# Performance work log

Hardware: AMD Instinct MI355X
Metric: run time of the kernel (lower is better)

## Reference

```python
import jax, jax.numpy as jnp
import numpy as np
from jax import lax

FEAT_X, FEAT_Y = 50, 37          # generate_anchors(50, 37)
BASE_SIZE, DSR = 8.0, 16.0
A = FEAT_X * FEAT_Y * 9          # 16650 anchors


def generate_anchors():
    # Vectorized version of the triple python loop; order: x, y, size, [b1,b2,b3]
    xs = jnp.arange(FEAT_X, dtype=jnp.float32)[:, None, None]
    ys = jnp.arange(FEAT_Y, dtype=jnp.float32)[None, :, None]
    s = jnp.array([BASE_SIZE, 2 * BASE_SIZE, 4 * BASE_SIZE], jnp.float32)[None, None, :]

    def box(x1, y1, x2, y2):
        return jnp.stack(jnp.broadcast_arrays(x1 * DSR, y1 * DSR, x2 * DSR, y2 * DSR), axis=-1)

    b1 = box(xs - s / 2, ys - s / 2, xs + s / 2, ys + s / 2)      # square
    b2 = box(xs - s,     ys - s / 4, xs + s,     ys + s / 4)      # wide
    b3 = box(xs - s / 4, ys - s,     xs + s / 4, ys + s)          # tall
    anchors = jnp.stack([b1, b2, b3], axis=3)  # (50,37,3 sizes,3 variants,4)
    return anchors.reshape(-1, 4)              # (16650,4)


def conv2d(x, w, b, padding):
    y = lax.conv_general_dilated(x, w, (1, 1), padding,
                                 dimension_numbers=("NCHW", "OIHW", "NCHW"))
    return y + b[None, :, None, None]


def pairwise_iou(anchors, gt):
    # anchors: (A,4), gt: (B,G,4) -> iou (B,A,G); zero when no positive overlap
    a = anchors[None, :, None, :]
    g = gt[:, None, :, :]
    area_a = (a[..., 2] - a[..., 0]) * (a[..., 3] - a[..., 1])
    area_g = (g[..., 2] - g[..., 0]) * (g[..., 3] - g[..., 1])
    left = jnp.maximum(a[..., 0], g[..., 0])
    right = jnp.minimum(a[..., 2], g[..., 2])
    top = jnp.maximum(a[..., 1], g[..., 1])
    bot = jnp.minimum(a[..., 3], g[..., 3])
    no_ov = (left >= right) | (top >= bot)
    inter = jnp.where(no_ov, 0.0, (right - left) * (bot - top))
    return jnp.where(no_ov, 0.0, inter / (area_a + area_g - inter))


def setup_inputs() -> dict:
    key = jax.random.key(0)
    k1, k2, k3, k4, k5, k6, k7, k8 = jax.random.split(key, 8)
    B, G = 8, 20
    feats = jax.random.normal(k1, (B, 512, FEAT_Y, FEAT_X), jnp.float32)
    # well-formed gt boxes inside an ~800x592 image
    raw = jax.random.uniform(k2, (B, G, 2, 2)) * jnp.array([800.0, 592.0])
    x1y1 = jnp.min(raw, axis=2)
    x2y2 = jnp.max(raw, axis=2) + 1.0
    gt_boxes = jnp.concatenate([x1y1, x2y2], axis=-1)  # (B,G,4)
    im_info = jnp.array([[592.0, 800.0, 1.0]], jnp.float32)  # (h, w, scale)
    s = 0.02
    w3 = jax.random.normal(k3, (512, 512, 3, 3), jnp.float32) * s
    b3 = jnp.zeros((512,), jnp.float32)
    wc = jax.random.normal(k4, (18, 512, 1, 1), jnp.float32) * s
    bc = jnp.zeros((18,), jnp.float32)
    wb = jax.random.normal(k5, (36, 512, 1, 1), jnp.float32) * s
    bb = jnp.zeros((36,), jnp.float32)
    return {"feats": feats, "w3": w3, "b3": b3, "wc": wc, "bc": bc,
            "wb": wb, "bb": bb, "gt_boxes": gt_boxes, "im_info": im_info}


def reference(feats, w3, b3, wc, bc, wb, bb, gt_boxes, im_info):
    B = feats.shape[0]
    anchors = generate_anchors()
    rpn_conv1 = jax.nn.relu(conv2d(feats, w3, b3, ((1, 1), (1, 1))))
    rpn_cls_score = conv2d(rpn_conv1, wc, bc, ((0, 0), (0, 0)))  # (B,18,H,W)
    Bc, C, H, W = rpn_cls_score.shape
    score_rs = rpn_cls_score.reshape(Bc, 2, (C * H) // 2, W)      # reshape(x, 2)
    rpn_cls_prob = jax.nn.softmax(score_rs, axis=1).reshape(Bc, 18, H, W)
    rpn_bbox_pred = conv2d(rpn_conv1, wb, bb, ((0, 0), (0, 0)))   # (B,36,H,W)

    # anchor-target assignment (training branch), faithful to original logic
    inside = ((anchors[:, 0] >= 0) & (anchors[:, 1] >= 0) &
              (anchors[:, 2] < im_info[0, 1]) & (anchors[:, 3] < im_info[0, 0]))
    iou = pairwise_iou(anchors, gt_boxes)                 # (B,A,G)
    iou = jnp.where(inside[None, :, None], iou, 0.0)      # outside anchors skipped
    G = gt_boxes.shape[1]
    # original: idxs = argmax(iou_matrix[:][j]) with j == last gt index
    idx = jnp.argmax(iou[:, G - 1, :], axis=-1)           # (B,)
    labels = jnp.zeros((B, anchors.shape[0]), jnp.float32)
    labels = labels.at[jnp.arange(B), idx].set(1.0)
    max_iou = jnp.max(iou, axis=-1)                       # (B,A)
    labels = jnp.where(inside[None, :] & (max_iou > 0.7), 0.0, labels)

    out = jnp.concatenate([rpn_cls_prob, rpn_bbox_pred], axis=1)  # (B,54,H,W)
    return out, iou, labels
```

## Files before the change

### kernel.cpp

```cpp
#include <hip/hip_runtime.h>

typedef unsigned short u16;
typedef unsigned int u32;
typedef float f32x4 __attribute__((ext_vector_type(4)));
typedef short bf16x8 __attribute__((ext_vector_type(8)));

#define NB 8
#define FH 37
#define FW 50
#define FHW 1850
#define MTOT 14800
#define CIN 512
#define KTOT 4608
#define HP 39
#define WP 52
#define ANCH 16650
#define NG 20

__device__ __forceinline__ u16 f2bf(float f) {
    u32 u = __float_as_uint(f);
    u += 0x7fffu + ((u >> 16) & 1u);
    return (u16)(u >> 16);
}

__device__ __forceinline__ void gl2lds16(const u16* g, u16* l) {
    __builtin_amdgcn_global_load_lds((const __attribute__((address_space(1))) void*)(g),
                                     (__attribute__((address_space(3))) void*)(l),
                                     16, 0, 0);
}

__device__ __forceinline__ void anchor_box(int a, float& x1, float& y1, float& x2, float& y2) {
    int x = a / 333;
    int rem = a - x * 333;
    int y = rem / 9;
    int r2 = rem - y * 9;
    int si = r2 / 3;
    int bi = r2 - si * 3;
    float s = (float)(8 << si);
    float fx = (float)x, fy = (float)y;
    float ax1, ay1, ax2, ay2;
    if (bi == 0)      { float h = s * 0.5f;  ax1 = fx - h; ay1 = fy - h; ax2 = fx + h; ay2 = fy + h; }
    else if (bi == 1) { float q = s * 0.25f; ax1 = fx - s; ay1 = fy - q; ax2 = fx + s; ay2 = fy + q; }
    else              { float q = s * 0.25f; ax1 = fx - q; ay1 = fy - s; ax2 = fx + q; ay2 = fy + s; }
    x1 = ax1 * 16.f; y1 = ay1 * 16.f; x2 = ax2 * 16.f; y2 = ay2 * 16.f;
}

__global__ void k_prep(uint4* __restrict__ apad4, const float* __restrict__ w3,
                       u16* __restrict__ wt, const float* __restrict__ wc,
                       const float* __restrict__ wb, u16* __restrict__ whd) {
    int bx = blockIdx.x;
    int t = threadIdx.x;
    if (bx < 4056) {
        apad4[bx * 256 + t] = make_uint4(0u, 0u, 0u, 0u);
    } else if (bx < 13272) {
        int i = (bx - 4056) * 256 + t;
        int n = i / KTOT;
        int k = i - n * KTOT;
        int tap = k >> 9;
        int ci = k & 511;
        wt[i] = f2bf(w3[n * KTOT + ci * 9 + tap]);
    } else {
        int i = (bx - 13272) * 256 + t;
        int n = i >> 9;
        int ci = i & 511;
        float v = 0.f;
        if (n < 18) v = wc[n * 512 + ci];
        else if (n < 54) v = wb[(n - 18) * 512 + ci];
        whd[i] = f2bf(v);
    }
}

__global__ void k_transpose(const float* __restrict__ feats, u16* __restrict__ apad) {
    __shared__ float tile[32][33];
    int b  = blockIdx.z;
    int hw0 = blockIdx.x * 32;
    int c0  = blockIdx.y * 32;
    int tx = threadIdx.x, ty = threadIdx.y;
    int hw = hw0 + tx;
    if (hw < FHW) tile[ty][tx] = feats[(b * 512 + c0 + ty) * FHW + hw];
    __syncthreads();
    int hw2 = hw0 + ty;
    if (hw2 < FHW) {
        int h = hw2 / FW, w = hw2 - h * FW;
        apad[(((b * HP) + h + 1) * WP + (w + 1)) * 512 + c0 + tx] = f2bf(tile[tx][ty]);
    }
}

__global__ __launch_bounds__(256) void k_conv(const u16* __restrict__ apad,
                                              const u16* __restrict__ wt,
                                              const float* __restrict__ b3,
                                              u16* __restrict__ act) {
    __shared__ u16 As[128 * 64];
    __shared__ u16 Bs[64 * 64];
    int tid = threadIdx.x;
    int wave = tid >> 6, lane = tid & 63;
    int m0 = blockIdx.x * 128;
    int n0 = blockIdx.y * 64;
    int wr = wave >> 1, wn = wave & 1;
    int lm = lane & 15, lq = lane >> 4;
    int l7 = lm & 7;

    f32x4 acc[4][2] = {};

    int rloc = tid >> 3;
    int cg = (tid & 7) ^ (rloc & 7);
    int aBase[4], bBase[2];
    for (int i = 0; i < 4; i++) {
        int m = m0 + i * 32 + rloc; if (m > MTOT - 1) m = MTOT - 1;
        int b = m / FHW; int hw = m - b * FHW;
        int h = hw / FW; int w = hw - h * FW;
        aBase[i] = ((b * HP + h) * WP + w) * 512 + cg * 8;
    }
    for (int j = 0; j < 2; j++)
        bBase[j] = (n0 + j * 32 + rloc) * KTOT + cg * 8;

    u16* aL[4]; u16* bL[2];
    for (int i = 0; i < 4; i++) aL[i] = &As[(i * 32 + wave * 8) * 64];
    for (int j = 0; j < 2; j++) bL[j] = &Bs[(j * 32 + wave * 8) * 64];

    for (int kk = 0; kk < KTOT; kk += 64) {
        int tap = kk >> 9;
        int ci0 = kk & 511;
        int dy = tap / 3, dx = tap - dy * 3;
        int aOfs = (dy * WP + dx) * 512 + ci0;
        gl2lds16(apad + aBase[0] + aOfs, aL[0]);
        gl2lds16(apad + aBase[1] + aOfs, aL[1]);
        gl2lds16(apad + aBase[2] + aOfs, aL[2]);
        gl2lds16(apad + aBase[3] + aOfs, aL[3]);
        gl2lds16(wt + bBase[0] + kk, bL[0]);
        gl2lds16(wt + bBase[1] + kk, bL[1]);
        __syncthreads();
        bf16x8 a[2][4], b[2][2];
        #pragma unroll
        for (int ks = 0; ks < 2; ks++) {
            int slotb = ((ks * 4 + lq) ^ l7) * 8;
            #pragma unroll
            for (int i = 0; i < 4; i++)
                a[ks][i] = *(const bf16x8*)&As[(wr * 64 + i * 16 + lm) * 64 + slotb];
            #pragma unroll
            for (int j = 0; j < 2; j++)
                b[ks][j] = *(const bf16x8*)&Bs[(wn * 32 + j * 16 + lm) * 64 + slotb];
        }
        #pragma unroll
        for (int ks = 0; ks < 2; ks++)
            #pragma unroll
            for (int i = 0; i < 4; i++)
                #pragma unroll
                for (int j = 0; j < 2; j++)
                    acc[i][j] = __builtin_amdgcn_mfma_f32_16x16x32_bf16(a[ks][i], b[ks][j], acc[i][j], 0, 0, 0);
        __syncthreads();
    }

    for (int j = 0; j < 2; j++) {
        int n = n0 + wn * 32 + j * 16 + lm;
        float bias = b3[n];
        for (int i = 0; i < 4; i++) {
            int mb = m0 + wr * 64 + i * 16 + lq * 4;
            for (int r = 0; r < 4; r++) {
                int m = mb + r;
                if (m < MTOT) {
                    float v = acc[i][j][r] + bias;
                    act[m * 512 + n] = f2bf(v > 0.f ? v : 0.f);
                }
            }
        }
    }
}

__global__ __launch_bounds__(256) void k_heads(const u16* __restrict__ act,
                                               const u16* __restrict__ whd,
                                               float* __restrict__ S) {
    int tid = threadIdx.x;
    int wave = tid >> 6, lane = tid & 63;
    int lm = lane & 15, lq = lane >> 4;
    int m0 = blockIdx.x * 64 + wave * 16;
    int mr = m0 + lm; if (mr > MTOT - 1) mr = MTOT - 1;
    const u16* arow = act + mr * 512;
    f32x4 acc[4] = {};
    for (int kk = 0; kk < 512; kk += 32) {
        bf16x8 a = *(const bf16x8*)&arow[kk + lq * 8];
        #pragma unroll
        for (int j = 0; j < 4; j++) {
            bf16x8 b = *(const bf16x8*)&whd[(j * 16 + lm) * 512 + kk + lq * 8];
            acc[j] = __builtin_amdgcn_mfma_f32_16x16x32_bf16(a, b, acc[j], 0, 0, 0);
        }
    }
    #pragma unroll
    for (int r = 0; r < 4; r++) {
        int m = m0 + lq * 4 + r;
        if (m < MTOT)
            for (int j = 0; j < 4; j++)
                S[m * 64 + j * 16 + lm] = acc[j][r];
    }
}

__global__ void k_final(const float* __restrict__ S, const float* __restrict__ bc,
                        const float* __restrict__ bb, float* __restrict__ out) {
    int m = blockIdx.x * 256 + threadIdx.x;
    if (m >= MTOT) return;
    int c = blockIdx.y;
    int b = m / FHW;
    int hw = m - b * FHW;
    float v;
    if (c < 18) {
        int c0 = c < 9 ? c : c - 9;
        float s0 = S[m * 64 + c0] + bc[c0];
        float s1 = S[m * 64 + c0 + 9] + bc[c0 + 9];
        float mx = fmaxf(s0, s1);
        float e0 = __expf(s0 - mx), e1 = __expf(s1 - mx);
        v = (c < 9 ? e0 : e1) / (e0 + e1);
    } else {
        v = S[m * 64 + c] + bb[c - 18];
    }
    out[(b * 54 + c) * FHW + hw] = v;
}

__global__ __launch_bounds__(256) void k_iou(const float* __restrict__ gt, const float* __restrict__ im,
                                             float* __restrict__ iou_out, float* __restrict__ lab) {
    __shared__ float g4[NG * 4];
    __shared__ float buf[256 * NG];
    __shared__ float imv[2];
    __shared__ int idxs;
    int t = threadIdx.x;
    int b = blockIdx.y;
    if (t < NG * 4) g4[t] = gt[b * NG * 4 + t];
    if (t < 2) imv[t] = im[t];
    __syncthreads();
    if (t == 0) {
        float x1, y1, x2, y2;
        anchor_box(19, x1, y1, x2, y2);
        bool inside = (x1 >= 0.f) && (y1 >= 0.f) && (x2 < imv[1]) && (y2 < imv[0]);
        float aa = (x2 - x1) * (y2 - y1);
        float best = -1.f; int bg = 0;
        for (int g = 0; g < NG; g++) {
            float gx1 = g4[g * 4], gy1 = g4[g * 4 + 1], gx2 = g4[g * 4 + 2], gy2 = g4[g * 4 + 3];
            float l = fmaxf(x1, gx1), r = fminf(x2, gx2);
            float tp = fmaxf(y1, gy1), bo = fminf(y2, gy2);
            float v = 0.f;
            if (l < r && tp < bo) {
                float inter = (r - l) * (bo - tp);
                float ag = (gx2 - gx1) * (gy2 - gy1);
                v = inter / (aa + ag - inter);
            }
            if (!inside) v = 0.f;
            if (v > best) { best = v; bg = g; }
        }
        idxs = bg;
    }
    int a0 = blockIdx.x * 256;
    int a = a0 + t;
    float mx = 0.f;
    bool inside = false;
    if (a < ANCH) {
        float x1, y1, x2, y2;
        anchor_box(a, x1, y1, x2, y2);
        inside = (x1 >= 0.f) && (y1 >= 0.f) && (x2 < imv[1]) && (y2 < imv[0]);
        float aa = (x2 - x1) * (y2 - y1);
        for (int g = 0; g < NG; g++) {
            float gx1 = g4[g * 4], gy1 = g4[g * 4 + 1], gx2 = g4[g * 4 + 2], gy2 = g4[g * 4 + 3];
            float l = fmaxf(x1, gx1), r = fminf(x2, gx2);
            float tp = fmaxf(y1, gy1), bo = fminf(y2, gy2);
            float v = 0.f;
            if (l < r && tp < bo) {
                float inter = (r - l) * (bo - tp);
                float ag = (gx2 - gx1) * (gy2 - gy1);
                v = inter / (aa + ag - inter);
            }
            if (!inside) v = 0.f;
            buf[t * NG + g] = v;
            mx = fmaxf(mx, v);
        }
    }
    __syncthreads();
    int rem = ANCH - a0;
    int cnt = (rem < 256 ? rem : 256) * NG;
    float* dst = iou_out + (b * ANCH + a0) * NG;
    for (int i = t; i < cnt; i += 256) dst[i] = buf[i];
    if (a < ANCH) {
        float lv = (a == idxs) ? 1.f : 0.f;
        if (inside && mx > 0.7f) lv = 0.f;
        lab[b * ANCH + a] = lv;
    }
}

extern "C" void kernel_launch(void* const* d_in, const int* in_sizes, int n_in,
                              void* d_out, int out_size, void* d_ws, size_t ws_size,
                              hipStream_t stream) {
    (void)in_sizes; (void)n_in; (void)out_size; (void)ws_size;
    const float* feats = (const float*)d_in[0];
    const float* w3    = (const float*)d_in[1];
    const float* b3    = (const float*)d_in[2];
    const float* wc    = (const float*)d_in[3];
    const float* bc    = (const float*)d_in[4];
    const float* wb    = (const float*)d_in[5];
    const float* bb    = (const float*)d_in[6];
    const float* gt    = (const float*)d_in[7];
    const float* im    = (const float*)d_in[8];
    float* out = (float*)d_out;
    char* ws = (char*)d_ws;

    u16* apad = (u16*)(ws);
    u16* wt   = (u16*)(ws + 16613376);
    u16* whd  = (u16*)(ws + 21331968);
    u16* act  = (u16*)(ws + 21397504);
    float* S  = (float*)(ws + 36552704);

    float* iou_out = out + 799200;
    float* lab     = out + 3463200;

    k_prep<<<dim3(13400), dim3(256), 0, stream>>>((uint4*)apad, w3, wt, wc, wb, whd);
    k_transpose<<<dim3(58, 16, 8), dim3(32, 32), 0, stream>>>(feats, apad);
    k_conv<<<dim3(116, 8), dim3(256), 0, stream>>>(apad, wt, b3, act);
    k_heads<<<dim3(232), dim3(256), 0, stream>>>(act, whd, S);
    k_final<<<dim3(58, 54), dim3(256), 0, stream>>>(S, bc, bb, out);
    k_iou<<<dim3(66, 8), dim3(256), 0, stream>>>(gt, im, iou_out, lab);
}
```

Baseline: 231.0 us.

## Merge prep, transpose and IoU kernels; fuse heads with softmax epilogue

```diff
diff --git a/kernel.cpp b/kernel.cpp
--- a/kernel.cpp
+++ b/kernel.cpp
@@ -16,6 +16,13 @@
 #define WP 52
 #define ANCH 16650
 #define NG 20
+
+#define ZB 356
+#define WTB 9216
+#define WHB 128
+#define TRB 7424
+#define IOB 528
+#define PRE_TOT (ZB + WTB + WHB + TRB + IOB)
 
 __device__ __forceinline__ u16 f2bf(float f) {
     u32 u = __float_as_uint(f);
@@ -45,44 +52,139 @@
     x1 = ax1 * 16.f; y1 = ay1 * 16.f; x2 = ax2 * 16.f; y2 = ay2 * 16.f;
 }
 
-__global__ void k_prep(uint4* __restrict__ apad4, const float* __restrict__ w3,
-                       u16* __restrict__ wt, const float* __restrict__ wc,
-                       const float* __restrict__ wb, u16* __restrict__ whd) {
-    int bx = blockIdx.x;
+__global__ __launch_bounds__(256) void k_pre(u16* __restrict__ apad,
+                                             const float* __restrict__ w3, u16* __restrict__ wt,
+                                             const float* __restrict__ wc, const float* __restrict__ wb,
+                                             u16* __restrict__ whd,
+                                             const float* __restrict__ feats,
+                                             const float* __restrict__ gt, const float* __restrict__ im,
+                                             float* __restrict__ iou_out, float* __restrict__ lab) {
+    __shared__ __attribute__((aligned(16))) char smraw[20864];
+    __shared__ int idxs;
+    int blk = blockIdx.x;
     int t = threadIdx.x;
-    if (bx < 4056) {
-        apad4[bx * 256 + t] = make_uint4(0u, 0u, 0u, 0u);
-    } else if (bx < 13272) {
-        int i = (bx - 4056) * 256 + t;
+
+    if (blk < ZB) {
+        uint4* apad4 = (uint4*)apad;
+        int i = blk * 256 + t;
+        int img = i / 11392;
+        int r = i - img * 11392;
+        int u4;
+        if (r < 3328) u4 = r;
+        else if (r < 6656) u4 = 126464 + (r - 3328);
+        else {
+            int rp = r - 6656;
+            int h = 1 + (rp >> 7);
+            int c2 = rp & 127;
+            int col = (c2 & 64) ? 51 : 0;
+            u4 = (h * 52 + col) * 64 + (c2 & 63);
+        }
+        apad4[img * 129792 + u4] = make_uint4(0u, 0u, 0u, 0u);
+    } else if (blk < ZB + WTB) {
+        int i = (blk - ZB) * 256 + t;
         int n = i / KTOT;
         int k = i - n * KTOT;
         int tap = k >> 9;
         int ci = k & 511;
         wt[i] = f2bf(w3[n * KTOT + ci * 9 + tap]);
-    } else {
-        int i = (bx - 13272) * 256 + t;
+    } else if (blk < ZB + WTB + WHB) {
+        int i = (blk - ZB - WTB) * 256 + t;
         int n = i >> 9;
         int ci = i & 511;
         float v = 0.f;
         if (n < 18) v = wc[n * 512 + ci];
         else if (n < 54) v = wb[(n - 18) * 512 + ci];
         whd[i] = f2bf(v);
-    }
-}
-
-__global__ void k_transpose(const float* __restrict__ feats, u16* __restrict__ apad) {
-    __shared__ float tile[32][33];
-    int b  = blockIdx.z;
-    int hw0 = blockIdx.x * 32;
-    int c0  = blockIdx.y * 32;
-    int tx = threadIdx.x, ty = threadIdx.y;
-    int hw = hw0 + tx;
-    if (hw < FHW) tile[ty][tx] = feats[(b * 512 + c0 + ty) * FHW + hw];
-    __syncthreads();
-    int hw2 = hw0 + ty;
-    if (hw2 < FHW) {
-        int h = hw2 / FW, w = hw2 - h * FW;
-        apad[(((b * HP) + h + 1) * WP + (w + 1)) * 512 + c0 + tx] = f2bf(tile[tx][ty]);
+    } else if (blk < ZB + WTB + WHB + TRB) {
+        float* tile = (float*)smraw;
+        int q = blk - ZB - WTB - WHB;
+        int xt = q % 58;
+        int r2 = q / 58;
+        int ct = r2 & 15;
+        int img = r2 >> 4;
+        int hw0 = xt * 32, c0 = ct * 32;
+        int tx = t & 31, ty4 = t >> 5;
+        #pragma unroll
+        for (int rr = 0; rr < 4; rr++) {
+            int ty = ty4 + rr * 8;
+            int hw = hw0 + tx;
+            if (hw < FHW) tile[ty * 33 + tx] = feats[(img * 512 + c0 + ty) * FHW + hw];
+        }
+        __syncthreads();
+        #pragma unroll
+        for (int rr = 0; rr < 4; rr++) {
+            int ty = ty4 + rr * 8;
+            int hw2 = hw0 + ty;
+            if (hw2 < FHW) {
+                int h = hw2 / FW, w = hw2 - h * FW;
+                apad[(((img * HP) + h + 1) * WP + (w + 1)) * 512 + c0 + tx] = f2bf(tile[tx * 33 + ty]);
+            }
+        }
+    } else {
+        float* g4 = (float*)smraw;
+        float* imv = g4 + 80;
+        float* buf = g4 + 84;
+        int q = blk - ZB - WTB - WHB - TRB;
+        int at = q % 66;
+        int b = q / 66;
+        if (t < NG * 4) g4[t] = gt[b * NG * 4 + t];
+        if (t < 2) imv[t] = im[t];
+        __syncthreads();
+        if (t == 0) {
+            float x1, y1, x2, y2;
+            anchor_box(19, x1, y1, x2, y2);
+            bool inside = (x1 >= 0.f) && (y1 >= 0.f) && (x2 < imv[1]) && (y2 < imv[0]);
+            float aa = (x2 - x1) * (y2 - y1);
+            float best = -1.f; int bg = 0;
+            for (int g = 0; g < NG; g++) {
+                float gx1 = g4[g * 4], gy1 = g4[g * 4 + 1], gx2 = g4[g * 4 + 2], gy2 = g4[g * 4 + 3];
+                float l = fmaxf(x1, gx1), r = fminf(x2, gx2);
+                float tp = fmaxf(y1, gy1), bo = fminf(y2, gy2);
+                float v = 0.f;
+                if (l < r && tp < bo) {
+                    float inter = (r - l) * (bo - tp);
+                    float ag = (gx2 - gx1) * (gy2 - gy1);
+                    v = inter / (aa + ag - inter);
+                }
+                if (!inside) v = 0.f;
+                if (v > best) { best = v; bg = g; }
+            }
+            idxs = bg;
+        }
+        int a0 = at * 256;
+        int a = a0 + t;
+        float mx = 0.f;
+        bool inside = false;
+        if (a < ANCH) {
+            float x1, y1, x2, y2;
+            anchor_box(a, x1, y1, x2, y2);
+            inside = (x1 >= 0.f) && (y1 >= 0.f) && (x2 < imv[1]) && (y2 < imv[0]);
+            float aa = (x2 - x1) * (y2 - y1);
+            for (int g = 0; g < NG; g++) {
+                float gx1 = g4[g * 4], gy1 = g4[g * 4 + 1], gx2 = g4[g * 4 + 2], gy2 = g4[g * 4 + 3];
+                float l = fmaxf(x1, gx1), r = fminf(x2, gx2);
+                float tp = fmaxf(y1, gy1), bo = fminf(y2, gy2);
+                float v = 0.f;
+                if (l < r && tp < bo) {
+                    float inter = (r - l) * (bo - tp);
+                    float ag = (gx2 - gx1) * (gy2 - gy1);
+                    v = inter / (aa + ag - inter);
+                }
+                if (!inside) v = 0.f;
+                buf[t * NG + g] = v;
+                mx = fmaxf(mx, v);
+            }
+        }
+        __syncthreads();
+        int rem = ANCH - a0;
+        int cnt = (rem < 256 ? rem : 256) * NG;
+        float* dst = iou_out + (b * ANCH + a0) * NG;
+        for (int i = t; i < cnt; i += 256) dst[i] = buf[i];
+        if (a < ANCH) {
+            float lv = (a == idxs) ? 1.f : 0.f;
+            if (inside && mx > 0.7f) lv = 0.f;
+            lab[b * ANCH + a] = lv;
+        }
     }
 }
 
@@ -92,10 +194,14 @@
                                               u16* __restrict__ act) {
     __shared__ u16 As[128 * 64];
     __shared__ u16 Bs[64 * 64];
+    int L = blockIdx.x;
+    int mb = (L & 7) + 8 * (L >> 6);
+    int nb = (L >> 3) & 7;
+    if (mb >= 116) return;
     int tid = threadIdx.x;
     int wave = tid >> 6, lane = tid & 63;
-    int m0 = blockIdx.x * 128;
-    int n0 = blockIdx.y * 64;
+    int m0 = mb * 128;
+    int n0 = nb * 64;
     int wr = wave >> 1, wn = wave & 1;
     int lm = lane & 15, lq = lane >> 4;
     int l7 = lm & 7;
@@ -155,9 +261,9 @@
         int n = n0 + wn * 32 + j * 16 + lm;
         float bias = b3[n];
         for (int i = 0; i < 4; i++) {
-            int mb = m0 + wr * 64 + i * 16 + lq * 4;
+            int mb2 = m0 + wr * 64 + i * 16 + lq * 4;
             for (int r = 0; r < 4; r++) {
-                int m = mb + r;
+                int m = mb2 + r;
                 if (m < MTOT) {
                     float v = acc[i][j][r] + bias;
                     act[m * 512 + n] = f2bf(v > 0.f ? v : 0.f);
@@ -167,9 +273,12 @@
     }
 }
 
-__global__ __launch_bounds__(256) void k_heads(const u16* __restrict__ act,
-                                               const u16* __restrict__ whd,
-                                               float* __restrict__ S) {
+__global__ __launch_bounds__(256) void k_post(const u16* __restrict__ act,
+                                              const u16* __restrict__ whd,
+                                              const float* __restrict__ bc,
+                                              const float* __restrict__ bb,
+                                              float* __restrict__ out) {
+    __shared__ float Sl[4 * 16 * 65];
     int tid = threadIdx.x;
     int wave = tid >> 6, lane = tid & 63;
     int lm = lane & 15, lq = lane >> 4;
@@ -185,101 +294,35 @@
             acc[j] = __builtin_amdgcn_mfma_f32_16x16x32_bf16(a, b, acc[j], 0, 0, 0);
         }
     }
+    float* S = &Sl[wave * 1040];
     #pragma unroll
-    for (int r = 0; r < 4; r++) {
-        int m = m0 + lq * 4 + r;
-        if (m < MTOT)
-            for (int j = 0; j < 4; j++)
-                S[m * 64 + j * 16 + lm] = acc[j][r];
-    }
-}
-
-__global__ void k_final(const float* __restrict__ S, const float* __restrict__ bc,
-                        const float* __restrict__ bb, float* __restrict__ out) {
-    int m = blockIdx.x * 256 + threadIdx.x;
-    if (m >= MTOT) return;
-    int c = blockIdx.y;
-    int b = m / FHW;
-    int hw = m - b * FHW;
-    float v;
-    if (c < 18) {
-        int c0 = c < 9 ? c : c - 9;
-        float s0 = S[m * 64 + c0] + bc[c0];
-        float s1 = S[m * 64 + c0 + 9] + bc[c0 + 9];
-        float mx = fmaxf(s0, s1);
-        float e0 = __expf(s0 - mx), e1 = __expf(s1 - mx);
-        v = (c < 9 ? e0 : e1) / (e0 + e1);
-    } else {
-        v = S[m * 64 + c] + bb[c - 18];
-    }
-    out[(b * 54 + c) * FHW + hw] = v;
-}
-
-__global__ __launch_bounds__(256) void k_iou(const float* __restrict__ gt, const float* __restrict__ im,
-                                             float* __restrict__ iou_out, float* __restrict__ lab) {
-    __shared__ float g4[NG * 4];
-    __shared__ float buf[256 * NG];
-    __shared__ float imv[2];
-    __shared__ int idxs;
-    int t = threadIdx.x;
-    int b = blockIdx.y;
-    if (t < NG * 4) g4[t] = gt[b * NG * 4 + t];
-    if (t < 2) imv[t] = im[t];
+    for (int r = 0; r < 4; r++)
+        #pragma unroll
+        for (int j = 0; j < 4; j++)
+            S[(lq * 4 + r) * 65 + j * 16 + lm] = acc[j][r];
     __syncthreads();
-    if (t == 0) {
-        float x1, y1, x2, y2;
-        anchor_box(19, x1, y1, x2, y2);
-        bool inside = (x1 >= 0.f) && (y1 >= 0.f) && (x2 < imv[1]) && (y2 < imv[0]);
-        float aa = (x2 - x1) * (y2 - y1);
-        float best = -1.f; int bg = 0;
-        for (int g = 0; g < NG; g++) {
-            float gx1 = g4[g * 4], gy1 = g4[g * 4 + 1], gx2 = g4[g * 4 + 2], gy2 = g4[g * 4 + 3];
-            float l = fmaxf(x1, gx1), r = fminf(x2, gx2);
-            float tp = fmaxf(y1, gy1), bo = fminf(y2, gy2);
-            float v = 0.f;
-            if (l < r && tp < bo) {
-                float inter = (r - l) * (bo - tp);
-                float ag = (gx2 - gx1) * (gy2 - gy1);
-                v = inter / (aa + ag - inter);
-            }
-            if (!inside) v = 0.f;
-            if (v > best) { best = v; bg = g; }
-        }
-        idxs = bg;
-    }
-    int a0 = blockIdx.x * 256;
-    int a = a0 + t;
-    float mx = 0.f;
-    bool inside = false;
-    if (a < ANCH) {
-        float x1, y1, x2, y2;
-        anchor_box(a, x1, y1, x2, y2);
-        inside = (x1 >= 0.f) && (y1 >= 0.f) && (x2 < imv[1]) && (y2 < imv[0]);
-        float aa = (x2 - x1) * (y2 - y1);
-        for (int g = 0; g < NG; g++) {
-            float gx1 = g4[g * 4], gy1 = g4[g * 4 + 1], gx2 = g4[g * 4 + 2], gy2 = g4[g * 4 + 3];
-            float l = fmaxf(x1, gx1), r = fminf(x2, gx2);
-            float tp = fmaxf(y1, gy1), bo = fminf(y2, gy2);
-            float v = 0.f;
-            if (l < r && tp < bo) {
-                float inter = (r - l) * (bo - tp);
-                float ag = (gx2 - gx1) * (gy2 - gy1);
-                v = inter / (aa + ag - inter);
-            }
-            if (!inside) v = 0.f;
-            buf[t * NG + g] = v;
-            mx = fmaxf(mx, v);
-        }
-    }
-    __syncthreads();
-    int rem = ANCH - a0;
-    int cnt = (rem < 256 ? rem : 256) * NG;
-    float* dst = iou_out + (b * ANCH + a0) * NG;
-    for (int i = t; i < cnt; i += 256) dst[i] = buf[i];
-    if (a < ANCH) {
-        float lv = (a == idxs) ? 1.f : 0.f;
-        if (inside && mx > 0.7f) lv = 0.f;
-        lab[b * ANCH + a] = lv;
+    int r16 = lane & 15, cg = lane >> 4;
+    int m = m0 + r16;
+    if (m < MTOT) {
+        int b = m / FHW, hw = m - b * FHW;
+        const float* Sr = &S[r16 * 65];
+        #pragma unroll
+        for (int k = 0; k < 14; k++) {
+            int c = cg + 4 * k;
+            if (c >= 54) break;
+            float v;
+            if (c < 18) {
+                int c0 = c < 9 ? c : c - 9;
+                float s0 = Sr[c0] + bc[c0];
+                float s1 = Sr[c0 + 9] + bc[c0 + 9];
+                float mx = fmaxf(s0, s1);
+                float e0 = __expf(s0 - mx), e1 = __expf(s1 - mx);
+                v = (c < 9 ? e0 : e1) / (e0 + e1);
+            } else {
+                v = Sr[c] + bb[c - 18];
+            }
+            out[(b * 54 + c) * FHW + hw] = v;
+        }
     }
 }
 
@@ -303,15 +346,12 @@
     u16* wt   = (u16*)(ws + 16613376);
     u16* whd  = (u16*)(ws + 21331968);
     u16* act  = (u16*)(ws + 21397504);
-    float* S  = (float*)(ws + 36552704);
 
     float* iou_out = out + 799200;
     float* lab     = out + 3463200;
 
-    k_prep<<<dim3(13400), dim3(256), 0, stream>>>((uint4*)apad, w3, wt, wc, wb, whd);
-    k_transpose<<<dim3(58, 16, 8), dim3(32, 32), 0, stream>>>(feats, apad);
-    k_conv<<<dim3(116, 8), dim3(256), 0, stream>>>(apad, wt, b3, act);
-    k_heads<<<dim3(232), dim3(256), 0, stream>>>(act, whd, S);
-    k_final<<<dim3(58, 54), dim3(256), 0, stream>>>(S, bc, bb, out);
-    k_iou<<<dim3(66, 8), dim3(256), 0, stream>>>(gt, im, iou_out, lab);
-}
+    k_pre<<<dim3(PRE_TOT), dim3(256), 0, stream>>>(apad, w3, wt, wc, wb, whd,
+                                                   feats, gt, im, iou_out, lab);
+    k_conv<<<dim3(960), dim3(256), 0, stream>>>(apad, wt, b3, act);
+    k_post<<<dim3(232), dim3(256), 0, stream>>>(act, whd, bc, bb, out);
+}
```

Result: faster. 210.3 us (-9.0%).
